# Performance work log

Measured on AMD Instinct MI355X. Metric: run time of the kernel, lower is better.

## Reference

```python
import jax, jax.numpy as jnp
import numpy as np

NUM_EXPERTS = 64
TOPK = 8
EPS = 1.1920929e-07  # torch.finfo(float32).eps


def setup_inputs() -> dict:
    key = jax.random.key(0)
    k1, k2 = jax.random.split(key)
    hidden_states = jax.random.normal(k1, (1, 4096, 4096), dtype=jnp.float32)
    wg_weight = jax.random.normal(k2, (NUM_EXPERTS, 4096), dtype=jnp.float32) * 0.02
    return {"hidden_states": hidden_states, "wg_weight": wg_weight}


def _routing(logits, capacity):
    # logits: [T, E]; capacity: static python int
    gates = jax.nn.softmax(logits, axis=1)                       # [T, E]
    _, idx = jax.lax.top_k(gates, TOPK)                          # [T, k]
    emask = jax.nn.one_hot(idx, NUM_EXPERTS, dtype=jnp.float32)  # [T, k, E]
    # sum of selected gate probs per token, clamped at fp32 eps
    gates_s = jnp.clip(jnp.einsum('tke,te->t', emask, gates), EPS)[:, None]
    router_probs = gates / gates_s                               # [T, E]
    # priority: cumulative position of each token within each expert,
    # scanned over (topk-major, token-minor) flattened order
    idx_flat = idx.T.reshape(-1)                                 # [k*T]
    mflat = jax.nn.one_hot(idx_flat, NUM_EXPERTS, dtype=jnp.int32)
    tp = jnp.cumsum(mflat, axis=0) * mflat - 1                   # [k*T, E]
    tp = tp.reshape(TOPK, -1, NUM_EXPERTS).transpose(1, 0, 2).max(axis=1)  # [T, E]
    valid = (tp >= 0) & (tp < capacity)                          # [T, E]
    tp = jnp.where(valid, tp, 0)
    dispatch_mask = jax.nn.one_hot(tp, capacity, dtype=jnp.bool_) & valid[:, :, None]  # [T, E, C]
    combine_weights = router_probs[:, :, None] * dispatch_mask   # [T, E, C]
    return combine_weights, dispatch_mask


def reference(hidden_states, wg_weight):
    b, s, h = hidden_states.shape
    x = hidden_states.reshape(-1, h).astype(jnp.float32)         # [T, H]
    logits = x @ wg_weight.T                                     # [T, E]
    # expert_capacity = max tokens assigned to any expert (data-dependent,
    # computed eagerly as in the torch .item() call)
    _, idx = jax.lax.top_k(jax.nn.softmax(logits, axis=1), TOPK)
    counts = jnp.bincount(idx.reshape(-1), length=NUM_EXPERTS)
    capacity = int(counts.max())
    return _routing(logits, capacity)
```

## Files before the change

### kernel.cpp

```cpp
#include <hip/hip_runtime.h>
#include <hip/hip_bf16.h>


#define TOK 4096
#define HID 4096
#define NE  64
#define NK  8

__global__ __launch_bounds__(256) void gemm_logits(
    const float* __restrict__ x, const float* __restrict__ wg,
    double* __restrict__ logits) {
  __shared__ float xs[16][68];
  __shared__ float wsh[64][68];
  const int tid = threadIdx.x;
  const int t0  = blockIdx.x * 16;
  const int tok = tid & 15;
  const int eg  = tid >> 4;
  const int lrow = tid >> 4;
  const int lq   = tid & 15;
  double acc[4] = {0.0, 0.0, 0.0, 0.0};

  for (int k0 = 0; k0 < HID; k0 += 64) {
    {
      float4 v = *(const float4*)&x[(size_t)(t0 + lrow) * HID + k0 + lq * 4];
      *(float4*)&xs[lrow][lq * 4] = v;
    }
#pragma unroll
    for (int it = 0; it < 4; ++it) {
      int r = it * 16 + lrow;
      float4 v = *(const float4*)&wg[(size_t)r * HID + k0 + lq * 4];
      *(float4*)&wsh[r][lq * 4] = v;
    }
    __syncthreads();
#pragma unroll
    for (int kk = 0; kk < 64; kk += 4) {
      float4 xv = *(const float4*)&xs[tok][kk];
#pragma unroll
      for (int j = 0; j < 4; ++j) {
        float4 wv = *(const float4*)&wsh[eg * 4 + j][kk];
        acc[j] = fma((double)xv.x, (double)wv.x, acc[j]);
        acc[j] = fma((double)xv.y, (double)wv.y, acc[j]);
        acc[j] = fma((double)xv.z, (double)wv.z, acc[j]);
        acc[j] = fma((double)xv.w, (double)wv.w, acc[j]);
      }
    }
    __syncthreads();
  }
#pragma unroll
  for (int j = 0; j < 4; ++j)
    logits[(size_t)(t0 + tok) * NE + eg * 4 + j] = acc[j];
}

__global__ __launch_bounds__(256) void topk_kernel(
    const double* __restrict__ logits,
    int* __restrict__ idx_kt, float* __restrict__ w_kt) {
  const int gid  = blockIdx.x * blockDim.x + threadIdx.x;
  const int t    = gid >> 6;
  const int lane = gid & 63;

  double v = logits[(size_t)t * NE + lane];
  double m = v;
#pragma unroll
  for (int off = 32; off; off >>= 1) {
    double o = __shfl_xor(m, off);
    m = o > m ? o : m;
  }
  double g = exp(v - m);
  double s = g;
#pragma unroll
  for (int off = 32; off; off >>= 1) s += __shfl_xor(s, off);
  double gate = g / s;

  float key = (float)gate;
  double ssel = 0.0;
  int my_k = -1;
#pragma unroll
  for (int k = 0; k < NK; ++k) {
    float bv = key;
    int   bi = lane;
#pragma unroll
    for (int off = 32; off; off >>= 1) {
      float ov = __shfl_xor(bv, off);
      int   oi = __shfl_xor(bi, off);
      if (ov > bv || (ov == bv && oi < bi)) { bv = ov; bi = oi; }
    }
    ssel += __shfl(gate, bi);
    if (lane == bi) { my_k = k; key = -1.0f; }
  }
  double gs = ssel;
  const double eps = (double)1.1920929e-07f;
  if (gs < eps) gs = eps;

  if (my_k >= 0) {
    idx_kt[my_k * TOK + t] = lane;
    w_kt [my_k * TOK + t] = (float)(gate / gs);
  }
}

__global__ __launch_bounds__(256) void rank_kernel(
    const int* __restrict__ idx_kt, int* __restrict__ rank_kt) {
  const int e    = blockIdx.x;
  const int tid  = threadIdx.x;
  const int lane = tid & 63;
  const int w    = tid >> 6;
  __shared__ int wt[4];
  int running = 0;
  const unsigned long long below = (1ull << lane) - 1ull;

  for (int i0 = 0; i0 < NK * TOK; i0 += 256) {
    const int i = i0 + tid;
    const bool mhit = (idx_kt[i] == e);
    unsigned long long mask = __ballot(mhit);
    if (lane == 0) wt[w] = __popcll(mask);
    __syncthreads();
    int woff = 0, tot = 0;
#pragma unroll
    for (int j = 0; j < 4; ++j) {
      int c = wt[j];
      tot += c;
      if (j < w) woff += c;
    }
    if (mhit) rank_kt[i] = running + woff + __popcll(mask & below);
    running += tot;
    __syncthreads();
  }
}

__global__ __launch_bounds__(256) void scatter_kernel(
    const int* __restrict__ idx_kt, const int* __restrict__ rank_kt,
    const float* __restrict__ w_kt, float* __restrict__ out, int C) {
  const int i = blockIdx.x * 256 + threadIdx.x;
  const int t = i & (TOK - 1);
  const int e = idx_kt[i];
  const int c = rank_kt[i];
  const float wv = w_kt[i];
  if (e >= 0 && e < NE && c >= 0 && c < C) {
    size_t off = ((size_t)t * NE + e) * (size_t)C + (size_t)c;
    out[off] = wv;
    out[(size_t)TOK * NE * C + off] = 1.0f;
  }
}

extern "C" void kernel_launch(void* const* d_in, const int* in_sizes, int n_in,
                              void* d_out, int out_size, void* d_ws, size_t ws_size,
                              hipStream_t stream) {
  const float* x  = (const float*)d_in[0];
  const float* wg = (const float*)d_in[1];
  float* out = (float*)d_out;

  const int C = out_size / (2 * TOK * NE);

  char* ws = (char*)d_ws;
  double* logits = (double*)ws;
  int*    idx_kt = (int*)  (ws + (size_t)2 * 1024 * 1024);
  int*    rank_kt= (int*)  (ws + (size_t)2 * 1024 * 1024 + 131072);
  float*  w_kt   = (float*)(ws + (size_t)2 * 1024 * 1024 + 2 * 131072);

  hipMemsetAsync(d_out, 0, (size_t)out_size * sizeof(float), stream);

  gemm_logits  <<<TOK / 16, 256, 0, stream>>>(x, wg, logits);
  topk_kernel  <<<TOK * 64 / 256, 256, 0, stream>>>(logits, idx_kt, w_kt);
  rank_kernel  <<<NE, 256, 0, stream>>>(idx_kt, rank_kt);
  scatter_kernel<<<NK * TOK / 256, 256, 0, stream>>>(idx_kt, rank_kt, w_kt, out, C);
}
```

Baseline: 1.355 ms.

## Compute gate logits with FP64 MFMA and split-K partial sums

Replaces the scalar FP64 FMA logits GEMM with a 64-token tile kernel that uses the f64 16x16x4 MFMA instruction. It probes the MFMA output layout at runtime to work out where each result belongs. The K dimension is split across up to eight blocks, which write partial slabs that topk_kernel sums. A sampled verify kernel checks the result, and a slow fallback repair GEMM runs if the check flags a layout mismatch. This adds workspace traffic for the partial slabs and two extra launches.

```diff
diff --git a/kernel.cpp b/kernel.cpp
--- a/kernel.cpp
+++ b/kernel.cpp
@@ -7,58 +7,126 @@
 #define NE  64
 #define NK  8
 
-__global__ __launch_bounds__(256) void gemm_logits(
+typedef double v4d __attribute__((ext_vector_type(4)));
+
+__global__ __launch_bounds__(256) void gemm_logits_mfma(
     const float* __restrict__ x, const float* __restrict__ wg,
-    double* __restrict__ logits) {
-  __shared__ float xs[16][68];
+    double* __restrict__ partial, int kchunk) {
+  __shared__ float xs[64][68];
   __shared__ float wsh[64][68];
-  const int tid = threadIdx.x;
-  const int t0  = blockIdx.x * 16;
-  const int tok = tid & 15;
-  const int eg  = tid >> 4;
-  const int lrow = tid >> 4;
-  const int lq   = tid & 15;
-  double acc[4] = {0.0, 0.0, 0.0, 0.0};
-
-  for (int k0 = 0; k0 < HID; k0 += 64) {
-    {
-      float4 v = *(const float4*)&x[(size_t)(t0 + lrow) * HID + k0 + lq * 4];
-      *(float4*)&xs[lrow][lq * 4] = v;
-    }
-#pragma unroll
-    for (int it = 0; it < 4; ++it) {
-      int r = it * 16 + lrow;
-      float4 v = *(const float4*)&wg[(size_t)r * HID + k0 + lq * 4];
-      *(float4*)&wsh[r][lq * 4] = v;
-    }
-    __syncthreads();
-#pragma unroll
-    for (int kk = 0; kk < 64; kk += 4) {
-      float4 xv = *(const float4*)&xs[tok][kk];
-#pragma unroll
-      for (int j = 0; j < 4; ++j) {
-        float4 wv = *(const float4*)&wsh[eg * 4 + j][kk];
-        acc[j] = fma((double)xv.x, (double)wv.x, acc[j]);
-        acc[j] = fma((double)xv.y, (double)wv.y, acc[j]);
-        acc[j] = fma((double)xv.z, (double)wv.z, acc[j]);
-        acc[j] = fma((double)xv.w, (double)wv.w, acc[j]);
-      }
-    }
-    __syncthreads();
-  }
-#pragma unroll
-  for (int j = 0; j < 4; ++j)
-    logits[(size_t)(t0 + tok) * NE + eg * 4 + j] = acc[j];
+  const int tid  = threadIdx.x;
+  const int lane = tid & 63;
+  const int w    = tid >> 6;
+  const int m16  = lane & 15;
+  const int q    = lane >> 4;
+  const int t0   = blockIdx.x * 64;
+  const int k0   = blockIdx.y * kchunk;
+
+  v4d pr = {0.0, 0.0, 0.0, 0.0};
+  v4d pc = pr;
+  pr = __builtin_amdgcn_mfma_f64_16x16x4f64((double)lane, 1.0, pr, 0, 0, 0);
+  pc = __builtin_amdgcn_mfma_f64_16x16x4f64(1.0, (double)lane, pc, 0, 0, 0);
+  int rmap[4], cmap[4];
+#pragma unroll
+  for (int v = 0; v < 4; ++v) {
+    int rv = (((int)(pr[v] + 0.5)) - 96) >> 2;
+    int cv = (((int)(pc[v] + 0.5)) - 96) >> 2;
+    rmap[v] = rv < 0 ? 0 : (rv > 15 ? 15 : rv);
+    cmap[v] = cv < 0 ? 0 : (cv > 15 ? 15 : cv);
+  }
+
+  v4d acc0 = {0.0, 0.0, 0.0, 0.0};
+  v4d acc1 = acc0, acc2 = acc0, acc3 = acc0;
+
+  const int lrow = tid >> 2;
+  const int lcol = (tid & 3) * 16;
+
+  for (int s = 0; s < kchunk; s += 64) {
+    const int kk0 = k0 + s;
+#pragma unroll
+    for (int j = 0; j < 4; ++j) {
+      *(float4*)&xs [lrow][lcol + j * 4] =
+          *(const float4*)&x [(size_t)(t0 + lrow) * HID + kk0 + lcol + j * 4];
+      *(float4*)&wsh[lrow][lcol + j * 4] =
+          *(const float4*)&wg[(size_t)lrow * HID + kk0 + lcol + j * 4];
+    }
+    __syncthreads();
+#pragma unroll
+    for (int s4 = 0; s4 < 16; ++s4) {
+      const int kr = s4 * 4 + q;
+      double a  = (double)xs [w * 16 + m16][kr];
+      double b0 = (double)wsh[ 0 + m16][kr];
+      double b1 = (double)wsh[16 + m16][kr];
+      double b2 = (double)wsh[32 + m16][kr];
+      double b3 = (double)wsh[48 + m16][kr];
+      acc0 = __builtin_amdgcn_mfma_f64_16x16x4f64(a, b0, acc0, 0, 0, 0);
+      acc1 = __builtin_amdgcn_mfma_f64_16x16x4f64(a, b1, acc1, 0, 0, 0);
+      acc2 = __builtin_amdgcn_mfma_f64_16x16x4f64(a, b2, acc2, 0, 0, 0);
+      acc3 = __builtin_amdgcn_mfma_f64_16x16x4f64(a, b3, acc3, 0, 0, 0);
+    }
+    __syncthreads();
+  }
+
+  double* base = partial + (size_t)blockIdx.y * TOK * NE;
+#pragma unroll
+  for (int v = 0; v < 4; ++v) {
+    const int row = t0 + w * 16 + rmap[v];
+    const int col = cmap[v];
+    double* rp = base + (size_t)row * NE;
+    rp[ 0 + col] = acc0[v];
+    rp[16 + col] = acc1[v];
+    rp[32 + col] = acc2[v];
+    rp[48 + col] = acc3[v];
+  }
+}
+
+__global__ __launch_bounds__(256) void verify_kernel(
+    const float* __restrict__ x, const float* __restrict__ wg,
+    const double* __restrict__ partial, int nsplit, int* __restrict__ flag) {
+  const int gid  = blockIdx.x * blockDim.x + threadIdx.x;
+  const int wid  = gid >> 6;
+  const int lane = gid & 63;
+  const int t = (wid * 521) & (TOK - 1);
+  const int e = wid & 63;
+  double acc = 0.0;
+  for (int k = lane; k < HID; k += 64)
+    acc = fma((double)x[(size_t)t * HID + k], (double)wg[(size_t)e * HID + k], acc);
+#pragma unroll
+  for (int off = 32; off; off >>= 1) acc += __shfl_xor(acc, off);
+  if (lane == 0) {
+    double got = 0.0;
+    for (int p = 0; p < nsplit; ++p)
+      got += partial[(size_t)p * TOK * NE + (size_t)t * NE + e];
+    if (!(fabs(got - acc) <= 1e-6)) atomicOr(flag, 1);
+  }
+}
+
+__global__ __launch_bounds__(256) void repair_gemm(
+    const float* __restrict__ x, const float* __restrict__ wg,
+    double* __restrict__ partial, int nsplit, const int* __restrict__ flag) {
+  if (*(volatile const int*)flag == 0) return;
+  const int gid = blockIdx.x * 256 + threadIdx.x;
+  const int t = gid >> 6;
+  const int e = gid & 63;
+  double acc = 0.0;
+  for (int k = 0; k < HID; ++k)
+    acc = fma((double)x[(size_t)t * HID + k], (double)wg[(size_t)e * HID + k], acc);
+  partial[(size_t)t * NE + e] = acc;
+  for (int p = 1; p < nsplit; ++p)
+    partial[(size_t)p * TOK * NE + (size_t)t * NE + e] = 0.0;
 }
 
 __global__ __launch_bounds__(256) void topk_kernel(
-    const double* __restrict__ logits,
+    const double* __restrict__ partial, int nsplit,
     int* __restrict__ idx_kt, float* __restrict__ w_kt) {
   const int gid  = blockIdx.x * blockDim.x + threadIdx.x;
   const int t    = gid >> 6;
   const int lane = gid & 63;
 
-  double v = logits[(size_t)t * NE + lane];
+  double v = 0.0;
+  for (int p = 0; p < nsplit; ++p)
+    v += partial[(size_t)p * TOK * NE + (size_t)t * NE + lane];
+
   double m = v;
 #pragma unroll
   for (int off = 32; off; off >>= 1) {
@@ -150,16 +218,27 @@
 
   const int C = out_size / (2 * TOK * NE);
 
+  const size_t slab = (size_t)TOK * NE * sizeof(double);
+  const size_t tail = 3 * (size_t)NK * TOK * sizeof(int);
+  int nsplit = 8;
+  while (nsplit > 1 && (size_t)nsplit * slab + tail + 64 > ws_size) nsplit >>= 1;
+  const int kchunk = HID / nsplit;
+
   char* ws = (char*)d_ws;
-  double* logits = (double*)ws;
-  int*    idx_kt = (int*)  (ws + (size_t)2 * 1024 * 1024);
-  int*    rank_kt= (int*)  (ws + (size_t)2 * 1024 * 1024 + 131072);
-  float*  w_kt   = (float*)(ws + (size_t)2 * 1024 * 1024 + 2 * 131072);
+  double* partial = (double*)ws;
+  int*    idx_kt  = (int*)  (ws + (size_t)nsplit * slab);
+  int*    rank_kt = (int*)  (ws + (size_t)nsplit * slab + (size_t)NK * TOK * 4);
+  float*  w_kt    = (float*)(ws + (size_t)nsplit * slab + (size_t)NK * TOK * 8);
+  int*    flag    = (int*)  (ws + (size_t)nsplit * slab + tail);
 
   hipMemsetAsync(d_out, 0, (size_t)out_size * sizeof(float), stream);
-
-  gemm_logits  <<<TOK / 16, 256, 0, stream>>>(x, wg, logits);
-  topk_kernel  <<<TOK * 64 / 256, 256, 0, stream>>>(logits, idx_kt, w_kt);
-  rank_kernel  <<<NE, 256, 0, stream>>>(idx_kt, rank_kt);
-  scatter_kernel<<<NK * TOK / 256, 256, 0, stream>>>(idx_kt, rank_kt, w_kt, out, C);
-}
+  hipMemsetAsync(flag, 0, sizeof(int), stream);
+
+  dim3 ggrid(TOK / 64, nsplit);
+  gemm_logits_mfma<<<ggrid, 256, 0, stream>>>(x, wg, partial, kchunk);
+  verify_kernel   <<<128, 256, 0, stream>>>(x, wg, partial, nsplit, flag);
+  repair_gemm     <<<TOK * NE / 256, 256, 0, stream>>>(x, wg, partial, nsplit, flag);
+  topk_kernel     <<<TOK * 64 / 256, 256, 0, stream>>>(partial, nsplit, idx_kt, w_kt);
+  rank_kernel     <<<NE, 256, 0, stream>>>(idx_kt, rank_kt);
+  scatter_kernel  <<<NK * TOK / 256, 256, 0, stream>>>(idx_kt, rank_kt, w_kt, out, C);
+}
```

After: 1.283 ms. 1.06x faster.

## Fuse output zero-fill into GEMM launch and widen rank kernel blocks

Applied to the files above, without the earlier changes.

Replaces the separate memset with extra blocks in the GEMM launch that zero the output using float4 stores, so the fill can overlap with the logits GEMM. Adds a sampled verify kernel and a flag-gated fallback GEMM that recomputes the logits if sampled values disagree. Also raises the rank kernel to 1024 threads per block to cut the number of serial scan iterations per expert. This adds two extra launches and a flag dependency. The out_size>>2 fill assumes out_size is divisible by 4.

```diff
diff --git a/kernel.cpp b/kernel.cpp
--- a/kernel.cpp
+++ b/kernel.cpp
@@ -6,13 +6,27 @@
 #define HID 4096
 #define NE  64
 #define NK  8
-
-__global__ __launch_bounds__(256) void gemm_logits(
+#define GEMMB 256
+#define FILLB 2048
+
+__global__ __launch_bounds__(256) void fused_gemm_fill(
     const float* __restrict__ x, const float* __restrict__ wg,
-    double* __restrict__ logits) {
+    double* __restrict__ logits, float* __restrict__ out, size_t n4,
+    int* __restrict__ flag) {
   __shared__ float xs[16][68];
   __shared__ float wsh[64][68];
   const int tid = threadIdx.x;
+
+  if ((int)blockIdx.x >= GEMMB) {
+    const int fb = (int)blockIdx.x - GEMMB;
+    const float4 z4 = make_float4(0.f, 0.f, 0.f, 0.f);
+    float4* o4 = (float4*)out;
+    for (size_t i = (size_t)fb * 256 + tid; i < n4; i += (size_t)FILLB * 256)
+      o4[i] = z4;
+    return;
+  }
+
+  if (blockIdx.x == 0 && tid == 0) *flag = 0;
   const int t0  = blockIdx.x * 16;
   const int tok = tid & 15;
   const int eg  = tid >> 4;
@@ -51,6 +65,52 @@
     logits[(size_t)(t0 + tok) * NE + eg * 4 + j] = acc[j];
 }
 
+__global__ __launch_bounds__(256) void verify_kernel(
+    const float* __restrict__ x, const float* __restrict__ wg,
+    const double* __restrict__ logits, int* __restrict__ flag) {
+  const int gid  = blockIdx.x * blockDim.x + threadIdx.x;
+  const int wid  = gid >> 6;
+  const int lane = gid & 63;
+  const int t = (wid * 521) & (TOK - 1);
+  const int e = wid & 63;
+  double acc = 0.0;
+  for (int k = lane; k < HID; k += 64)
+    acc = fma((double)x[(size_t)t * HID + k], (double)wg[(size_t)e * HID + k], acc);
+#pragma unroll
+  for (int off = 32; off; off >>= 1) acc += __shfl_xor(acc, off);
+  if (lane == 0) {
+    double got = logits[(size_t)t * NE + e];
+    if (!(fabs(got - acc) <= 1e-6)) atomicOr(flag, 1);
+  }
+}
+
+__global__ __launch_bounds__(256) void repair_gemm(
+    const float* __restrict__ x, const float* __restrict__ wg,
+    double* __restrict__ logits, const int* __restrict__ flag) {
+  if (*(volatile const int*)flag == 0) return;
+  const int gid = blockIdx.x * 256 + threadIdx.x;
+  const int t = gid >> 6;
+  const int e = gid & 63;
+  double a0 = 0, a1 = 0, a2 = 0, a3 = 0, a4 = 0, a5 = 0, a6 = 0, a7 = 0;
+  const float* xr = x  + (size_t)t * HID;
+  const float* wr = wg + (size_t)e * HID;
+  for (int k = 0; k < HID; k += 8) {
+    float4 xv0 = *(const float4*)&xr[k];
+    float4 xv1 = *(const float4*)&xr[k + 4];
+    float4 wv0 = *(const float4*)&wr[k];
+    float4 wv1 = *(const float4*)&wr[k + 4];
+    a0 = fma((double)xv0.x, (double)wv0.x, a0);
+    a1 = fma((double)xv0.y, (double)wv0.y, a1);
+    a2 = fma((double)xv0.z, (double)wv0.z, a2);
+    a3 = fma((double)xv0.w, (double)wv0.w, a3);
+    a4 = fma((double)xv1.x, (double)wv1.x, a4);
+    a5 = fma((double)xv1.y, (double)wv1.y, a5);
+    a6 = fma((double)xv1.z, (double)wv1.z, a6);
+    a7 = fma((double)xv1.w, (double)wv1.w, a7);
+  }
+  logits[(size_t)t * NE + e] = ((((((a0 + a1) + a2) + a3) + a4) + a5) + a6) + a7;
+}
+
 __global__ __launch_bounds__(256) void topk_kernel(
     const double* __restrict__ logits,
     int* __restrict__ idx_kt, float* __restrict__ w_kt) {
@@ -59,6 +119,7 @@
   const int lane = gid & 63;
 
   double v = logits[(size_t)t * NE + lane];
+
   double m = v;
 #pragma unroll
   for (int off = 32; off; off >>= 1) {
@@ -97,17 +158,17 @@
   }
 }
 
-__global__ __launch_bounds__(256) void rank_kernel(
+__global__ __launch_bounds__(1024) void rank_kernel(
     const int* __restrict__ idx_kt, int* __restrict__ rank_kt) {
   const int e    = blockIdx.x;
   const int tid  = threadIdx.x;
   const int lane = tid & 63;
   const int w    = tid >> 6;
-  __shared__ int wt[4];
+  __shared__ int wt[16];
   int running = 0;
   const unsigned long long below = (1ull << lane) - 1ull;
 
-  for (int i0 = 0; i0 < NK * TOK; i0 += 256) {
+  for (int i0 = 0; i0 < NK * TOK; i0 += 1024) {
     const int i = i0 + tid;
     const bool mhit = (idx_kt[i] == e);
     unsigned long long mask = __ballot(mhit);
@@ -115,7 +176,7 @@
     __syncthreads();
     int woff = 0, tot = 0;
 #pragma unroll
-    for (int j = 0; j < 4; ++j) {
+    for (int j = 0; j < 16; ++j) {
       int c = wt[j];
       tot += c;
       if (j < w) woff += c;
@@ -151,15 +212,18 @@
   const int C = out_size / (2 * TOK * NE);
 
   char* ws = (char*)d_ws;
-  double* logits = (double*)ws;
-  int*    idx_kt = (int*)  (ws + (size_t)2 * 1024 * 1024);
-  int*    rank_kt= (int*)  (ws + (size_t)2 * 1024 * 1024 + 131072);
-  float*  w_kt   = (float*)(ws + (size_t)2 * 1024 * 1024 + 2 * 131072);
-
-  hipMemsetAsync(d_out, 0, (size_t)out_size * sizeof(float), stream);
-
-  gemm_logits  <<<TOK / 16, 256, 0, stream>>>(x, wg, logits);
-  topk_kernel  <<<TOK * 64 / 256, 256, 0, stream>>>(logits, idx_kt, w_kt);
-  rank_kernel  <<<NE, 256, 0, stream>>>(idx_kt, rank_kt);
-  scatter_kernel<<<NK * TOK / 256, 256, 0, stream>>>(idx_kt, rank_kt, w_kt, out, C);
-}
+  double* logits  = (double*)ws;
+  int*    idx_kt  = (int*)  (ws + (size_t)2 * 1024 * 1024);
+  int*    rank_kt = (int*)  (ws + (size_t)2 * 1024 * 1024 + (size_t)NK * TOK * 4);
+  float*  w_kt    = (float*)(ws + (size_t)2 * 1024 * 1024 + (size_t)NK * TOK * 8);
+  int*    flag    = (int*)  (ws + (size_t)2 * 1024 * 1024 + (size_t)NK * TOK * 12);
+
+  const size_t n4 = (size_t)out_size >> 2;
+
+  fused_gemm_fill<<<GEMMB + FILLB, 256, 0, stream>>>(x, wg, logits, out, n4, flag);
+  verify_kernel  <<<128, 256, 0, stream>>>(x, wg, logits, flag);
+  repair_gemm    <<<TOK * NE / 256, 256, 0, stream>>>(x, wg, logits, flag);
+  topk_kernel    <<<TOK * 64 / 256, 256, 0, stream>>>(logits, idx_kt, w_kt);
+  rank_kernel    <<<NE, 1024, 0, stream>>>(idx_kt, rank_kt);
+  scatter_kernel <<<NK * TOK / 256, 256, 0, stream>>>(idx_kt, rank_kt, w_kt, out, C);
+}
```

Measured after the change: 1.316 ms. 2.9% less time.
